# Performance work log

Measured on AMD Instinct MI355X. Metric: run time of the kernel, lower is better.

## Reference

```python
import jax, jax.numpy as jnp
from jax import lax
import numpy as np

N, C_IN, C_OUT, H, W, DS = 32, 16, 1, 128, 128, 5
NC = C_OUT * C_IN  # channels fed to DUBlock convs (= out_nc*nc_d[0])


def autocorr(x, ds):
    """x:(N,C,H,W) -> xtx_raw:(N,C,C,2ds-1,2ds-1).
    xtx_raw[n,i,j,u,v] = sum_{h,w} x[n,i,h,w] * xpad[n,j,u+h,v+w]  (zero pad ds-1),
    matching torch cal_xtx (sample-wise conv3d of x with itself)."""
    n, c, h, w = x.shape
    p = ds - 1
    xp = jnp.pad(x, ((0, 0), (0, 0), (p, p), (p, p)))
    rows = []
    for u in range(2 * ds - 1):
        cols = [jnp.einsum('nihw,njhw->nij', x,
                           lax.slice(xp, (0, 0, u, v), (n, c, u + h, v + w)))
                for v in range(2 * ds - 1)]
        rows.append(jnp.stack(cols, axis=-1))
    return jnp.stack(rows, axis=-2)  # (N,C,C,K,K), K=2ds-1


def crosscorr(x, y, ds):
    """x:(N,Ci,H,W), y:(N,Co,H,W) -> xty:(N,Co,Ci,ds,ds)  (torch cal_xty, pad=(ds-1)//2)."""
    n, c, h, w = x.shape
    p = (ds - 1) // 2
    xp = jnp.pad(x, ((0, 0), (0, 0), (p, p), (p, p)))
    rows = []
    for u in range(ds):
        cols = [jnp.einsum('nohw,njhw->noj', y,
                           lax.slice(xp, (0, 0, u, v), (n, c, u + h, v + w)))
                for v in range(ds)]
        rows.append(jnp.stack(cols, axis=-1))
    return jnp.stack(rows, axis=-2)  # (N,Co,Ci,ds,ds)


def assemble_Q(R, ds):
    """Block-Toeplitz assembly. Equivalent to torch's unfold + flip + index permutation:
    Q[n,(i,p,q),(j,oi,oj)] = R[n,i,j, ds-1+oi-p, ds-1+oj-q]."""
    n, c = R.shape[0], R.shape[1]
    r = jnp.arange(ds)
    idx = (ds - 1) + r[None, :] - r[:, None]  # idx[p,o] = ds-1+o-p in [0, 2ds-2]
    Q6 = R[:, :, :, idx[:, None, :, None], idx[None, :, None, :]]  # (N,i,j,p,q,oi,oj)
    return jnp.transpose(Q6, (0, 1, 3, 4, 2, 5, 6)).reshape(n, c * ds * ds, c * ds * ds)


def dsb(x, d, y, alpha, reg):
    """DSBlock: regularized normal equations + batched SPD solve.
    x:(N,Ci,H,W), d:(N,Co,Ci,ds,ds), y:(N,Co,H,W), alpha:(N,1,1,1), reg:(1,)"""
    n, ci, h, w = x.shape
    co, ds = d.shape[1], d.shape[-1]
    Q = assemble_Q(autocorr(x, ds), ds)                               # (N, ci*ds^2, ci*ds^2)
    P = crosscorr(x, y, ds).reshape(n, co, -1).transpose(0, 2, 1)      # (N, ci*ds^2, co)
    a = alpha.reshape(n, 1, 1) * (h * w) * reg / (ds * ds * ci)        # (N,1,1)
    m = Q.shape[1]
    Q = Q + a * jnp.eye(m, dtype=Q.dtype)
    P = P + a * d.reshape(n, co, -1).transpose(0, 2, 1)
    # torch uses cholesky + cholesky_solve on SPD Q; jnp.linalg.solve computes the
    # same solution (and its vjp matches the custom CholeskySolve backward for symmetric Q).
    D = jnp.linalg.solve(Q, P)                                         # (N, ci*ds^2, co)
    return D.reshape(n, ci, ds, ds, co).transpose(0, 4, 1, 2, 3)       # (N,Co,Ci,ds,ds)


def conv3x3(x, wgt, b):
    o = lax.conv_general_dilated(x, wgt, (1, 1), ((1, 1), (1, 1)),
                                 dimension_numbers=('NCHW', 'OIHW', 'NCHW'))
    return o + b[None, :, None, None]


def dblock_fwd(x1, x2, d, y1, y2, alpha, beta, reg,
               w1, b1, w2, b2, w3, b3, w4, b4, w5, b5, w6, b6):
    d = dsb(x1, d, y1, alpha, reg)
    d = dsb(x2, d, y2, alpha, reg)
    n, co, ci, ds = d.shape[0], d.shape[1], d.shape[2], d.shape[3]
    bmap = jnp.broadcast_to(1.0 / jnp.sqrt(beta), (n, 1, ds, ds))      # (1/beta.sqrt()).repeat
    h0 = jnp.concatenate([d.reshape(n, co * ci, ds, ds), bmap], axis=1)
    # DUBlock
    t = jax.nn.relu(conv3x3(jax.nn.relu(conv3x3(h0, w1, b1)), w2, b2))
    t = jax.nn.relu(conv3x3(jax.nn.relu(conv3x3(t, w3, b3)), w4, b4))
    t = conv3x3(jax.nn.relu(conv3x3(t, w5, b5)), w6, b6) + h0[:, :-1]
    return t.reshape(n, co, ci, ds, ds)


def setup_inputs() -> dict:
    key = jax.random.key(0)
    ks = jax.random.split(key, 24)
    inp = {
        'x1': jax.random.normal(ks[0], (N, C_IN, H, W), jnp.float32),
        'x2': jax.random.normal(ks[1], (N, C_IN, H, W), jnp.float32),
        'd': jax.random.normal(ks[2], (N, C_OUT, C_IN, DS, DS), jnp.float32),
        'y1': jax.random.normal(ks[3], (N, C_OUT, H, W), jnp.float32),
        'y2': jax.random.normal(ks[4], (N, C_OUT, H, W), jnp.float32),
        'alpha': jax.random.uniform(ks[5], (N, 1, 1, 1), jnp.float32),
        'beta': jax.random.uniform(ks[6], (N, 1, 1, 1), jnp.float32),
        'reg': jnp.ones((1,), jnp.float32),
    }
    cins = [NC + 1, NC, NC, NC, NC, NC]
    for i in range(6):
        inp['w%d' % (i + 1)] = 0.05 * jax.random.normal(ks[7 + i], (NC, cins[i], 3, 3), jnp.float32)
        inp['b%d' % (i + 1)] = jnp.zeros((NC,), jnp.float32)
    return inp


def reference(x1, x2, d, y1, y2, alpha, beta, reg,
              w1, b1, w2, b2, w3, b3, w4, b4, w5, b5, w6, b6):
    return dblock_fwd(x1, x2, d, y1, y2, alpha, beta, reg,
                      w1, b1, w2, b2, w3, b3, w4, b4, w5, b5, w6, b6)
```

## Files before the change

kernel.cpp:

```cpp
#include <hip/hip_runtime.h>
#include <hip/hip_bf16.h>

constexpr int NS   = 32;
constexpr int C    = 16;
constexpr int H    = 128;
constexpr int W    = 128;
constexpr int DS   = 5;
constexpr int M    = C * DS * DS;
constexpr int NLAG = 81;

typedef short short8 __attribute__((ext_vector_type(8)));
typedef float f32x4 __attribute__((ext_vector_type(4)));

constexpr int CH_U    = 152;
constexpr int SLOT_U  = 16 * CH_U;
constexpr int SLOT_B  = SLOT_U * 2;
constexpr int RING_B  = 16 * SLOT_B;
constexpr int CHK     = 19;
constexpr size_t XB_US_PER_IN = (size_t)NS * H * 16 * CH_U;

constexpr int WREP_F  = 6 * 144 * 20 + 6 * 16;
constexpr int WREP_CH = WREP_F * 4 / 16;

__device__ __forceinline__ unsigned int pk_bf16(float a, float b) {
    union { __hip_bfloat162 h; unsigned int u; } cv;
    cv.h = __float22bfloat162_rn(make_float2(a, b));
    return cv.u;
}

__device__ __forceinline__ void gl_lds16(const void* g, void* l) {
    __builtin_amdgcn_global_load_lds(
        (const __attribute__((address_space(1))) unsigned int*)g,
        (__attribute__((address_space(3))) unsigned int*)l, 16, 0, 0);
}

__global__ __launch_bounds__(256, 1)
void prep_kernel(const float* __restrict__ x1, const float* __restrict__ x2,
                 const float* __restrict__ y1, const float* __restrict__ y2,
                 unsigned short* __restrict__ xb,
                 float* __restrict__ P1, float* __restrict__ P2,
                 const float* __restrict__ w1, const float* __restrict__ b1,
                 const float* __restrict__ w2, const float* __restrict__ b2,
                 const float* __restrict__ w3, const float* __restrict__ b3,
                 const float* __restrict__ w4, const float* __restrict__ b4,
                 const float* __restrict__ w5, const float* __restrict__ b5,
                 const float* __restrict__ w6, const float* __restrict__ b6,
                 float* __restrict__ wrep)
{
    const int b = blockIdx.x, tid = threadIdx.x;
    if (b < 1024) {
        const int n = b & 31, zi = (b >> 5) & 1, rg = b >> 6;
        const float* xn = (zi ? x2 : x1) + (size_t)n * C * H * W;
        uint4* dst = (uint4*)(xb + (size_t)zi * XB_US_PER_IN +
                              ((size_t)n * H) * SLOT_U);
        for (int f = tid; f < 8 * 16 * CHK; f += 256) {
            const int rc = f / CHK, g = f - rc * CHK;
            const int row = rg * 8 + (rc >> 4), ch = rc & 15;
            uint4 o = make_uint4(0u, 0u, 0u, 0u);
            if (g >= 1 && g <= 16) {
                const float4* s4 = (const float4*)(xn + ((size_t)ch * H + row) * W + (g - 1) * 8);
                float4 va = s4[0], vb = s4[1];
                o.x = pk_bf16(va.x, va.y); o.y = pk_bf16(va.z, va.w);
                o.z = pk_bf16(vb.x, vb.y); o.w = pk_bf16(vb.z, vb.w);
            }
            dst[((size_t)row * 16 + ch) * CHK + g] = o;
        }
        return;
    }
    if (b < 2048) {
        const int b2 = b - 1024;
        const int n = b2 & 31, j = (b2 >> 5) & 15, zi = b2 >> 9;
        const float* x = zi ? x2 : x1;
        const float* y = zi ? y2 : y1;
        float* P       = zi ? P2 : P1;

        const float* yn = y + (size_t)n * H * W;
        const float* xc = x + ((size_t)n * C + j) * H * W;

        const int wg = tid & 31, slab = tid >> 5;
        const int r0 = slab * 16;

        float acc[25];
#pragma unroll
        for (int l = 0; l < 25; ++l) acc[l] = 0.f;

        float4 yw[5];
#pragma unroll
        for (int u = 0; u < 5; ++u) {
            const int t = r0 + 1 - u;
            yw[u] = (t >= 0) ? *(const float4*)(yn + (size_t)t * W + wg * 4)
                             : make_float4(0.f, 0.f, 0.f, 0.f);
        }

#pragma unroll 4
        for (int rr = 0; rr < 16; ++rr) {
            const int r = r0 + rr;
#pragma unroll
            for (int u = 4; u >= 1; --u) yw[u] = yw[u - 1];
            const int tnew = r + 2;
            yw[0] = (tnew < H) ? *(const float4*)(yn + (size_t)tnew * W + wg * 4)
                               : make_float4(0.f, 0.f, 0.f, 0.f);

            const float* xr = xc + (size_t)r * W + wg * 4;
            float w12[12];
            float4 t4 = (wg > 0) ? *(const float4*)(xr - 4) : make_float4(0, 0, 0, 0);
            w12[0] = t4.x; w12[1] = t4.y; w12[2] = t4.z; w12[3] = t4.w;
            t4 = *(const float4*)(xr);
            w12[4] = t4.x; w12[5] = t4.y; w12[6] = t4.z; w12[7] = t4.w;
            t4 = (wg < 31) ? *(const float4*)(xr + 4) : make_float4(0, 0, 0, 0);
            w12[8] = t4.x; w12[9] = t4.y; w12[10] = t4.z; w12[11] = t4.w;

#pragma unroll
            for (int u = 0; u < 5; ++u) {
#pragma unroll
                for (int v = 0; v < 5; ++v)
                    acc[u * 5 + v] += yw[u].x * w12[2 + v] + yw[u].y * w12[3 + v] +
                                      yw[u].z * w12[4 + v] + yw[u].w * w12[5 + v];
            }
        }

        __shared__ float red[4][25];
        const int lane = tid & 63, wv = tid >> 6;
#pragma unroll
        for (int l = 0; l < 25; ++l) {
            float v = acc[l];
#pragma unroll
            for (int off = 32; off; off >>= 1) v += __shfl_down(v, off);
            if (lane == 0) red[wv][l] = v;
        }
        __syncthreads();
        if (tid < 25)
            P[((size_t)n * C + j) * 25 + tid] = red[0][tid] + red[1][tid] + red[2][tid] + red[3][tid];
        return;
    }
    const float* wsl[6] = {w1, w2, w3, w4, w5, w6};
    const float* bsl[6] = {b1, b2, b3, b4, b5, b6};
#pragma unroll
    for (int l = 0; l < 6; ++l) {
        const int cin = (l == 0) ? 17 : 16;
        const float* ws = wsl[l];
        for (int f = tid; f < 16 * cin * 9; f += 256) {
            const int o = f / (cin * 9);
            const int rm = f - o * cin * 9;
            const int ci = rm / 9, kk = rm - ci * 9;
            wrep[l * 2880 + (o * 9 + kk) * 20 + ci] = ws[f];
        }
        if (tid < 16) wrep[17280 + l * 16 + tid] = bsl[l][tid];
    }
}

template<int P0, int P1>
__device__ __forceinline__ void autocorr_body(const unsigned short* __restrict__ xn,
                                              float* __restrict__ Rn,
                                              char* sm, int tid)
{
    constexpr int U0 = P0 / 9;
    constexpr int U1 = (P1 - 1) / 9;
    constexpr int NB = U1 - U0 + 1;
    constexpr int NP = P1 - P0;
    constexpr int SLOT_Q = SLOT_B / 16;

    unsigned short* ring = (unsigned short*)sm;
    const int lane = tid & 63;
    const int wid  = tid >> 6;
    const int q    = lane >> 4;
    const int mi   = lane & 15;
    const int rh   = wid & 3;
    const int chh  = wid >> 2;

    f32x4 acc[NP];
#pragma unroll
    for (int l = 0; l < NP; ++l) acc[l] = (f32x4){0.f, 0.f, 0.f, 0.f};

    const char* gb = (const char*)xn;

    for (int f = tid; f < 4 * SLOT_Q; f += 512)
        ((uint4*)sm)[(12 + f / SLOT_Q) * SLOT_Q + (f % SLOT_Q)] = make_uint4(0, 0, 0, 0);
    for (int f = wid; f < 38; f += 8)
        gl_lds16(gb + (size_t)f * 1024 + lane * 16, sm + f * 1024);
    __syncthreads();

    for (int s = 0; s < H; s += 4) {
        if (s < H - 8) {
            const size_t gbase = (size_t)(s + 8) * SLOT_B;
            char* lbase = sm + ((s + 8) & 15) * SLOT_B;
            for (int f = wid; f < 19; f += 8)
                gl_lds16(gb + gbase + (size_t)f * 1024 + lane * 16, lbase + f * 1024);
        } else {
            for (int f = tid; f < 4 * SLOT_Q; f += 512)
                ((uint4*)sm)[(((s + 8 + f / SLOT_Q) & 15)) * SLOT_Q + (f % SLOT_Q)] = make_uint4(0, 0, 0, 0);
        }

        const int r = s + rh;
        const unsigned short* rowA = ring + (r & 15) * SLOT_U + mi * CH_U;
#pragma unroll
        for (int cc = 0; cc < 2; ++cc) {
            const int w0 = (chh * 2 + cc) * 32;
            const uint4* pa = (const uint4*)(rowA + w0 + 8 * q);
            uint4 A0 = pa[0], A1 = pa[1], A2 = pa[2];
            unsigned int d[12] = {A0.x, A0.y, A0.z, A0.w, A1.x, A1.y, A1.z, A1.w,
                                  A2.x, A2.y, A2.z, A2.w};
            short8 bf[NB];
#pragma unroll
            for (int u = U0; u <= U1; ++u)
                bf[u - U0] = *(const short8*)(ring + ((r + u - 4 + 16) & 15) * SLOT_U +
                                              mi * CH_U + 8 + w0 + 8 * q);
#pragma unroll
            for (int v = 0; v < 9; ++v) {
                const int off = 12 - v;
                const int q4  = off >> 1;
                union { unsigned int u4[4]; short8 s8; } af;
                if (off & 1) {
#pragma unroll
                    for (int k2 = 0; k2 < 4; ++k2)
                        af.u4[k2] = (d[q4 + k2] >> 16) | (d[q4 + k2 + 1] << 16);
                } else {
#pragma unroll
                    for (int k2 = 0; k2 < 4; ++k2) af.u4[k2] = d[q4 + k2];
                }
#pragma unroll
                for (int u = U0; u <= U1; ++u) {
                    if (u * 9 + v >= P0 && u * 9 + v < P1)
                        acc[u * 9 + v - P0] = __builtin_amdgcn_mfma_f32_16x16x32_bf16(
                            af.s8, bf[u - U0], acc[u * 9 + v - P0], 0, 0, 0);
                }
            }
        }
        __syncthreads();
    }

    float* sred = (float*)sm;
#pragma unroll
    for (int cb = 0; cb < NP; cb += 9) {
        const int nc = (NP - cb < 9) ? (NP - cb) : 9;
        __syncthreads();
#pragma unroll
        for (int pp = 0; pp < 9; ++pp) {
            if (pp < nc) {
#pragma unroll
                for (int rg = 0; rg < 4; ++rg)
                    sred[(pp * 8 + wid) * 256 + (q * 4 + rg) * 16 + mi] = acc[cb + pp][rg];
            }
        }
        __syncthreads();
        if (tid < 256) {
#pragma unroll
            for (int pp = 0; pp < 9; ++pp) {
                if (pp < nc) {
                    float ssum = 0.f;
#pragma unroll
                    for (int w8 = 0; w8 < 8; ++w8)
                        ssum += sred[(pp * 8 + w8) * 256 + tid];
                    Rn[(size_t)tid * NLAG + P0 + cb + pp] = ssum;
                }
            }
        }
    }
}

__global__ __launch_bounds__(512, 2)
void autocorr_mfma(const unsigned short* __restrict__ xb,
                   float* __restrict__ R1, float* __restrict__ R2)
{
    __shared__ __align__(16) char sm[RING_B];
    const int n = blockIdx.x, zi = blockIdx.y, ug = blockIdx.z;
    const unsigned short* xn = xb + (size_t)zi * XB_US_PER_IN + (size_t)n * H * SLOT_U;
    float* Rn = (zi ? R2 : R1) + (size_t)n * C * C * NLAG;
    switch (ug) {
        case 0:  autocorr_body< 0, 20>(xn, Rn, sm, threadIdx.x); break;
        case 1:  autocorr_body<20, 40>(xn, Rn, sm, threadIdx.x); break;
        case 2:  autocorr_body<40, 60>(xn, Rn, sm, threadIdx.x); break;
        default: autocorr_body<60, 81>(xn, Rn, sm, threadIdx.x); break;
    }
}

__device__ __forceinline__ float block_sum512(float v, float* red, int tid)
{
#pragma unroll
    for (int off = 32; off; off >>= 1) v += __shfl_down(v, off);
    if ((tid & 63) == 0) red[tid >> 6] = v;
    __syncthreads();
    float s = red[0] + red[1] + red[2] + red[3] + red[4] + red[5] + red[6] + red[7];
    __syncthreads();
    return s;
}

__device__ __forceinline__ float2 block_sum512_f2(float v0, float v1, float* red, int tid)
{
#pragma unroll
    for (int off = 32; off; off >>= 1) { v0 += __shfl_down(v0, off); v1 += __shfl_down(v1, off); }
    if ((tid & 63) == 0) { red[(tid >> 6) * 2] = v0; red[(tid >> 6) * 2 + 1] = v1; }
    __syncthreads();
    float s0 = 0.f, s1 = 0.f;
#pragma unroll
    for (int i = 0; i < 8; ++i) { s0 += red[2 * i]; s1 += red[2 * i + 1]; }
    __syncthreads();
    return make_float2(s0, s1);
}

__device__ __forceinline__ float cg_solve(const float (&Rreg)[81], float rhs,
                                          int iters, float a, int t,
                                          float* pv, float* ap, float* red)
{
    const int jj = t & 15;
    float zreg = 0.f, rreg = 0.f, pmine = 0.f;
    if (t < M) {
        rreg = rhs; pmine = rhs;
        pv[(t / 25) * 28 + (t % 25)] = rhs;
    }
    float rr = block_sum512((t < M) ? rreg * rreg : 0.f, red, t);

    for (int it = 0; it < iters; ++it) {
        if (t < 256) {
            float pld[25], acc[25];
            const float* pj = &pv[jj * 28];
#pragma unroll
            for (int k = 0; k < 25; ++k) pld[k] = pj[k];
#pragma unroll
            for (int k = 0; k < 25; ++k) acc[k] = 0.f;
#pragma unroll
            for (int u = 0; u < 9; ++u) {
#pragma unroll
                for (int v = 0; v < 9; ++v) {
                    const float Rv = Rreg[u * 9 + v];
#pragma unroll
                    for (int c = 0; c < 5; ++c) {
                        if (c < u - 4 || c > u) continue;
                        const int aa = 4 + c - u;
#pragma unroll
                        for (int dd = 0; dd < 5; ++dd) {
                            if (dd < v - 4 || dd > v) continue;
                            const int bb = 4 + dd - v;
                            acc[aa * 5 + bb] += Rv * pld[c * 5 + dd];
                        }
                    }
                }
            }
#pragma unroll
            for (int k = 0; k < 25; ++k) {
                float s2 = acc[k];
                s2 += __shfl_down(s2, 8, 16);
                s2 += __shfl_down(s2, 4, 16);
                s2 += __shfl_down(s2, 2, 16);
                s2 += __shfl_down(s2, 1, 16);
                acc[k] = s2;
            }
            if (jj == 0) {
#pragma unroll
                for (int k = 0; k < 25; ++k) ap[(t >> 4) * 25 + k] = acc[k];
            }
        }
        __syncthreads();
        float wv = 0.f;
        if (t < M) wv = ap[t] + a * pmine;
        const float2 dots = block_sum512_f2((t < M) ? pmine * wv : 0.f,
                                            (t < M) ? wv * wv : 0.f, red, t);
        const float pAp = dots.x, ww = dots.y;
        const bool ok = (pAp > 1e-30f);
        const float al  = ok ? rr / pAp : 0.f;
        float rrn = ok ? fmaxf(al * al * ww - rr, 0.f) : rr;
        const float be  = (rr > 1e-30f) ? rrn / rr : 0.f;
        rr = rrn;
        if (t < M) {
            zreg += al * pmine;
            rreg -= al * wv;
            pmine = rreg + be * pmine;
            pv[(t / 25) * 28 + (t % 25)] = pmine;
        }
        __syncthreads();
    }
    return zreg;
}

__global__ __launch_bounds__(512, 1)
void solve_kernel(const float* __restrict__ R1, const float* __restrict__ R2,
                  const float* __restrict__ P1, const float* __restrict__ P2,
                  const float* __restrict__ d0, const float* __restrict__ alpha,
                  const float* __restrict__ beta, const float* __restrict__ reg,
                  const float* __restrict__ wrep,
                  float* __restrict__ out)
{
    __shared__ __align__(16) float Rl[256 * NLAG];
    __shared__ float pv[16 * 28];
    __shared__ float ap[M];
    __shared__ float red[16];
    __shared__ float h0p[25 * 20];
    __shared__ float bufA[25 * 20], bufB[25 * 20];

    const int n = blockIdx.x, t = threadIdx.x;
    const float a = alpha[n] * (float)(H * W) * reg[0] / (float)(DS * DS * C);

    {
        const char* g = (const char*)(R1 + (size_t)n * 256 * NLAG);
        char* l = (char*)Rl;
        for (int f = t; f < 5184; f += 512)
            gl_lds16(g + (size_t)f * 16, l + (size_t)f * 16);
    }
    float rhs1 = 0.f;
    if (t < M) rhs1 = P1[(size_t)n * M + t] + a * d0[(size_t)n * M + t];
    __syncthreads();

    float Rreg[81];
    {
        const float* Rrow = &Rl[(t & 255) * NLAG];
#pragma unroll
        for (int i = 0; i < 81; ++i) Rreg[i] = Rrow[i];
    }
    __syncthreads();

    {
        const char* g = (const char*)(R2 + (size_t)n * 256 * NLAG);
        char* l = (char*)Rl;
        for (int f = t; f < 5184; f += 512)
            gl_lds16(g + (size_t)f * 16, l + (size_t)f * 16);
    }
    float z1 = cg_solve(Rreg, rhs1, 3, a, t, pv, ap, red);
    {
        const float* Rrow = &Rl[(t & 255) * NLAG];
#pragma unroll
        for (int i = 0; i < 81; ++i) Rreg[i] = Rrow[i];
    }
    __syncthreads();

    {
        const char* g = (const char*)wrep;
        char* l = (char*)Rl;
        for (int f = t; f < WREP_CH; f += 512)
            gl_lds16(g + (size_t)f * 16, l + (size_t)f * 16);
    }
    float rhs2 = 0.f;
    if (t < M) rhs2 = P2[(size_t)n * M + t] + a * z1;
    float z2 = cg_solve(Rreg, rhs2, 7, a, t, pv, ap, red);

    const float* wall = (const float*)Rl;
    if (t < M) h0p[(t % 25) * 20 + t / 25] = z2;
    if (t < 25) h0p[t * 20 + 16] = rsqrtf(beta[n]);
    __syncthreads();

#pragma unroll
    for (int l = 0; l < 6; ++l) {
        const float* act = (l == 0) ? h0p : ((l & 1) ? bufA : bufB);
        float s = 0.f;
        if (t < 400) {
            const int o = t / 25, pix = t % 25, yy = pix / 5, xx = pix % 5;
            s = wall[17280 + l * 16 + o];
#pragma unroll
            for (int ky = 0; ky < 3; ++ky) {
                const int iy = yy + ky - 1;
                if ((unsigned)iy >= 5u) continue;
#pragma unroll
                for (int kx = 0; kx < 3; ++kx) {
                    const int ix = xx + kx - 1;
                    if ((unsigned)ix >= 5u) continue;
                    const float* ip = act + (iy * 5 + ix) * 20;
                    const float* wp = wall + l * 2880 + (o * 9 + ky * 3 + kx) * 20;
                    const float4 a0 = *(const float4*)(ip);
                    const float4 a1 = *(const float4*)(ip + 4);
                    const float4 a2 = *(const float4*)(ip + 8);
                    const float4 a3 = *(const float4*)(ip + 12);
                    const float4 q0 = *(const float4*)(wp);
                    const float4 q1 = *(const float4*)(wp + 4);
                    const float4 q2 = *(const float4*)(wp + 8);
                    const float4 q3 = *(const float4*)(wp + 12);
                    s += a0.x * q0.x + a0.y * q0.y + a0.z * q0.z + a0.w * q0.w
                       + a1.x * q1.x + a1.y * q1.y + a1.z * q1.z + a1.w * q1.w
                       + a2.x * q2.x + a2.y * q2.y + a2.z * q2.z + a2.w * q2.w
                       + a3.x * q3.x + a3.y * q3.y + a3.z * q3.z + a3.w * q3.w;
                    if (l == 0) s += ip[16] * wp[16];
                }
            }
            if (l < 5) s = fmaxf(s, 0.f);
            else       s += h0p[(t % 25) * 20 + t / 25];
        }
        if (t < 400) {
            if (l == 5) out[(size_t)n * M + t] = s;
            else {
                float* dstb = (l & 1) ? bufB : bufA;
                dstb[(t % 25) * 20 + t / 25] = s;
            }
        }
        __syncthreads();
    }
}

extern "C" void kernel_launch(void* const* d_in, const int* in_sizes, int n_in,
                              void* d_out, int out_size, void* d_ws, size_t ws_size,
                              hipStream_t stream)
{
    (void)in_sizes; (void)n_in; (void)out_size; (void)ws_size;
    const float* x1    = (const float*)d_in[0];
    const float* x2    = (const float*)d_in[1];
    const float* d0    = (const float*)d_in[2];
    const float* y1    = (const float*)d_in[3];
    const float* y2    = (const float*)d_in[4];
    const float* alpha = (const float*)d_in[5];
    const float* beta  = (const float*)d_in[6];
    const float* reg   = (const float*)d_in[7];
    const float* w1 = (const float*)d_in[8];  const float* b1 = (const float*)d_in[9];
    const float* w2 = (const float*)d_in[10]; const float* b2 = (const float*)d_in[11];
    const float* w3 = (const float*)d_in[12]; const float* b3 = (const float*)d_in[13];
    const float* w4 = (const float*)d_in[14]; const float* b4 = (const float*)d_in[15];
    const float* w5 = (const float*)d_in[16]; const float* b5 = (const float*)d_in[17];
    const float* w6 = (const float*)d_in[18]; const float* b6 = (const float*)d_in[19];
    float* out = (float*)d_out;

    char* wsb = (char*)d_ws;
    unsigned short* xb = (unsigned short*)wsb;
    float* R1 = (float*)(wsb + 2 * XB_US_PER_IN * 2);
    const size_t RSZ = (size_t)NS * C * C * NLAG;
    float* R2 = R1 + RSZ;
    float* P1 = R2 + RSZ;
    float* P2 = P1 + (size_t)NS * M;
    float* wrep = P2 + (size_t)NS * M;

    prep_kernel<<<2049, 256, 0, stream>>>(x1, x2, y1, y2, xb, P1, P2,
                                          w1, b1, w2, b2, w3, b3, w4, b4,
                                          w5, b5, w6, b6, wrep);
    autocorr_mfma<<<dim3(NS, 2, 4), 512, 0, stream>>>(xb, R1, R2);
    solve_kernel<<<NS, 512, 0, stream>>>(R1, R2, P1, P2, d0, alpha, beta, reg,
                                         wrep, out);
}
```

Before: 291.1 us.

## Shrink solve kernel to 256 threads with two elements per thread

The solve kernel now runs 256 threads instead of 512, and each thread owns two of the 400 CG vector elements. Block reductions now span 4 waves instead of 8. The CG loop is restructured to compute pAp and the residual norm separately, and it skips the final residual/direction update. The pv row padding changes from 28 to 29 to reduce LDS bank conflicts. The aim is to cut barrier and reduction overhead in this latency-bound 32-block kernel, at the cost of more serial work per thread in the elementwise and conv stages.

```diff
diff --git a/kernel.cpp b/kernel.cpp
--- a/kernel.cpp
+++ b/kernel.cpp
@@ -21,6 +21,8 @@
 
 constexpr int WREP_F  = 6 * 144 * 20 + 6 * 16;
 constexpr int WREP_CH = WREP_F * 4 / 16;
+
+constexpr int PVP = 29;
 
 __device__ __forceinline__ unsigned int pk_bf16(float a, float b) {
     union { __hip_bfloat162 h; unsigned int u; } cv;
@@ -274,105 +276,125 @@
     }
 }
 
-__device__ __forceinline__ float block_sum512(float v, float* red, int tid)
+__device__ __forceinline__ float block_sum256(float v, float* red, int t)
 {
 #pragma unroll
     for (int off = 32; off; off >>= 1) v += __shfl_down(v, off);
-    if ((tid & 63) == 0) red[tid >> 6] = v;
-    __syncthreads();
-    float s = red[0] + red[1] + red[2] + red[3] + red[4] + red[5] + red[6] + red[7];
+    if ((t & 63) == 0) red[t >> 6] = v;
+    __syncthreads();
+    float s = red[0] + red[1] + red[2] + red[3];
     __syncthreads();
     return s;
 }
 
-__device__ __forceinline__ float2 block_sum512_f2(float v0, float v1, float* red, int tid)
-{
-#pragma unroll
-    for (int off = 32; off; off >>= 1) { v0 += __shfl_down(v0, off); v1 += __shfl_down(v1, off); }
-    if ((tid & 63) == 0) { red[(tid >> 6) * 2] = v0; red[(tid >> 6) * 2 + 1] = v1; }
-    __syncthreads();
-    float s0 = 0.f, s1 = 0.f;
-#pragma unroll
-    for (int i = 0; i < 8; ++i) { s0 += red[2 * i]; s1 += red[2 * i + 1]; }
-    __syncthreads();
-    return make_float2(s0, s1);
-}
-
-__device__ __forceinline__ float cg_solve(const float (&Rreg)[81], float rhs,
-                                          int iters, float a, int t,
-                                          float* pv, float* ap, float* red)
+__device__ __forceinline__ void cg_solve(const float (&Rreg)[81],
+                                         float rhs0, float rhs1,
+                                         int iters, float a, int t, bool has1,
+                                         float* pv, float* ap, float* red,
+                                         float& z0o, float& z1o)
 {
     const int jj = t & 15;
-    float zreg = 0.f, rreg = 0.f, pmine = 0.f;
-    if (t < M) {
-        rreg = rhs; pmine = rhs;
-        pv[(t / 25) * 28 + (t % 25)] = rhs;
-    }
-    float rr = block_sum512((t < M) ? rreg * rreg : 0.f, red, t);
+    const int e1 = t + 256;
+    float z0 = 0.f, z1 = 0.f;
+    float r0 = rhs0, r1 = has1 ? rhs1 : 0.f;
+    float p0 = r0, p1 = r1;
+    pv[(t / 25) * PVP + (t % 25)] = p0;
+    if (has1) pv[(e1 / 25) * PVP + (e1 % 25)] = p1;
+    float rr = block_sum256(r0 * r0 + r1 * r1, red, t);
 
     for (int it = 0; it < iters; ++it) {
-        if (t < 256) {
-            float pld[25], acc[25];
-            const float* pj = &pv[jj * 28];
-#pragma unroll
-            for (int k = 0; k < 25; ++k) pld[k] = pj[k];
-#pragma unroll
-            for (int k = 0; k < 25; ++k) acc[k] = 0.f;
-#pragma unroll
-            for (int u = 0; u < 9; ++u) {
-#pragma unroll
-                for (int v = 0; v < 9; ++v) {
-                    const float Rv = Rreg[u * 9 + v];
-#pragma unroll
-                    for (int c = 0; c < 5; ++c) {
-                        if (c < u - 4 || c > u) continue;
-                        const int aa = 4 + c - u;
-#pragma unroll
-                        for (int dd = 0; dd < 5; ++dd) {
-                            if (dd < v - 4 || dd > v) continue;
-                            const int bb = 4 + dd - v;
-                            acc[aa * 5 + bb] += Rv * pld[c * 5 + dd];
-                        }
+        float pld[25], acc[25];
+        const float* pj = &pv[jj * PVP];
+#pragma unroll
+        for (int k = 0; k < 25; ++k) pld[k] = pj[k];
+#pragma unroll
+        for (int k = 0; k < 25; ++k) acc[k] = 0.f;
+#pragma unroll
+        for (int u = 0; u < 9; ++u) {
+#pragma unroll
+            for (int v = 0; v < 9; ++v) {
+                const float Rv = Rreg[u * 9 + v];
+#pragma unroll
+                for (int c = 0; c < 5; ++c) {
+                    if (c < u - 4 || c > u) continue;
+                    const int aa = 4 + c - u;
+#pragma unroll
+                    for (int dd = 0; dd < 5; ++dd) {
+                        if (dd < v - 4 || dd > v) continue;
+                        const int bb = 4 + dd - v;
+                        acc[aa * 5 + bb] += Rv * pld[c * 5 + dd];
                     }
                 }
             }
-#pragma unroll
-            for (int k = 0; k < 25; ++k) {
-                float s2 = acc[k];
-                s2 += __shfl_down(s2, 8, 16);
-                s2 += __shfl_down(s2, 4, 16);
-                s2 += __shfl_down(s2, 2, 16);
-                s2 += __shfl_down(s2, 1, 16);
-                acc[k] = s2;
-            }
-            if (jj == 0) {
-#pragma unroll
-                for (int k = 0; k < 25; ++k) ap[(t >> 4) * 25 + k] = acc[k];
-            }
+        }
+#pragma unroll
+        for (int k = 0; k < 25; ++k) {
+            float s2 = acc[k];
+            s2 += __shfl_down(s2, 8, 16);
+            s2 += __shfl_down(s2, 4, 16);
+            s2 += __shfl_down(s2, 2, 16);
+            s2 += __shfl_down(s2, 1, 16);
+            acc[k] = s2;
+        }
+        if (jj == 0) {
+#pragma unroll
+            for (int k = 0; k < 25; ++k) ap[(t >> 4) * 25 + k] = acc[k];
         }
         __syncthreads();
-        float wv = 0.f;
-        if (t < M) wv = ap[t] + a * pmine;
-        const float2 dots = block_sum512_f2((t < M) ? pmine * wv : 0.f,
-                                            (t < M) ? wv * wv : 0.f, red, t);
-        const float pAp = dots.x, ww = dots.y;
-        const bool ok = (pAp > 1e-30f);
-        const float al  = ok ? rr / pAp : 0.f;
-        float rrn = ok ? fmaxf(al * al * ww - rr, 0.f) : rr;
-        const float be  = (rr > 1e-30f) ? rrn / rr : 0.f;
-        rr = rrn;
-        if (t < M) {
-            zreg += al * pmine;
-            rreg -= al * wv;
-            pmine = rreg + be * pmine;
-            pv[(t / 25) * 28 + (t % 25)] = pmine;
-        }
-        __syncthreads();
-    }
-    return zreg;
-}
-
-__global__ __launch_bounds__(512, 1)
+        const float w0 = ap[t] + a * p0;
+        const float w1 = has1 ? (ap[e1] + a * p1) : 0.f;
+        const float pAp = block_sum256(p0 * w0 + p1 * w1, red, t);
+        const float al  = (pAp > 1e-30f) ? rr / pAp : 0.f;
+        z0 += al * p0; z1 += al * p1;
+        if (it + 1 < iters) {
+            r0 -= al * w0; r1 -= al * w1;
+            const float rrn = block_sum256(r0 * r0 + r1 * r1, red, t);
+            const float be  = (rr > 1e-30f) ? rrn / rr : 0.f;
+            rr = rrn;
+            p0 = r0 + be * p0; p1 = r1 + be * p1;
+            pv[(t / 25) * PVP + (t % 25)] = p0;
+            if (has1) pv[(e1 / 25) * PVP + (e1 % 25)] = p1;
+            __syncthreads();
+        }
+    }
+    z0o = z0; z1o = z1;
+}
+
+__device__ __forceinline__ float conv_one(const float* __restrict__ act,
+                                          const float* __restrict__ wall,
+                                          int l, int idx)
+{
+    const int o = idx / 25, pix = idx % 25, yy = pix / 5, xx = pix % 5;
+    float s = wall[17280 + l * 16 + o];
+#pragma unroll
+    for (int ky = 0; ky < 3; ++ky) {
+        const int iy = yy + ky - 1;
+        if ((unsigned)iy >= 5u) continue;
+#pragma unroll
+        for (int kx = 0; kx < 3; ++kx) {
+            const int ix = xx + kx - 1;
+            if ((unsigned)ix >= 5u) continue;
+            const float* ip = act + (iy * 5 + ix) * 20;
+            const float* wp = wall + l * 2880 + (o * 9 + ky * 3 + kx) * 20;
+            const float4 a0 = *(const float4*)(ip);
+            const float4 a1 = *(const float4*)(ip + 4);
+            const float4 a2 = *(const float4*)(ip + 8);
+            const float4 a3 = *(const float4*)(ip + 12);
+            const float4 q0 = *(const float4*)(wp);
+            const float4 q1 = *(const float4*)(wp + 4);
+            const float4 q2 = *(const float4*)(wp + 8);
+            const float4 q3 = *(const float4*)(wp + 12);
+            s += a0.x * q0.x + a0.y * q0.y + a0.z * q0.z + a0.w * q0.w
+               + a1.x * q1.x + a1.y * q1.y + a1.z * q1.z + a1.w * q1.w
+               + a2.x * q2.x + a2.y * q2.y + a2.z * q2.z + a2.w * q2.w
+               + a3.x * q3.x + a3.y * q3.y + a3.z * q3.z + a3.w * q3.w;
+            if (l == 0) s += ip[16] * wp[16];
+        }
+    }
+    return s;
+}
+
+__global__ __launch_bounds__(256, 1)
 void solve_kernel(const float* __restrict__ R1, const float* __restrict__ R2,
                   const float* __restrict__ P1, const float* __restrict__ P2,
                   const float* __restrict__ d0, const float* __restrict__ alpha,
@@ -381,28 +403,30 @@
                   float* __restrict__ out)
 {
     __shared__ __align__(16) float Rl[256 * NLAG];
-    __shared__ float pv[16 * 28];
+    __shared__ float pv[16 * PVP];
     __shared__ float ap[M];
-    __shared__ float red[16];
+    __shared__ float red[8];
     __shared__ float h0p[25 * 20];
     __shared__ float bufA[25 * 20], bufB[25 * 20];
 
     const int n = blockIdx.x, t = threadIdx.x;
+    const bool has1 = (t < M - 256);
+    const int e1 = t + 256;
     const float a = alpha[n] * (float)(H * W) * reg[0] / (float)(DS * DS * C);
 
     {
         const char* g = (const char*)(R1 + (size_t)n * 256 * NLAG);
         char* l = (char*)Rl;
-        for (int f = t; f < 5184; f += 512)
+        for (int f = t; f < 5184; f += 256)
             gl_lds16(g + (size_t)f * 16, l + (size_t)f * 16);
     }
-    float rhs1 = 0.f;
-    if (t < M) rhs1 = P1[(size_t)n * M + t] + a * d0[(size_t)n * M + t];
+    const float rhs10 = P1[(size_t)n * M + t] + a * d0[(size_t)n * M + t];
+    const float rhs11 = has1 ? (P1[(size_t)n * M + e1] + a * d0[(size_t)n * M + e1]) : 0.f;
     __syncthreads();
 
     float Rreg[81];
     {
-        const float* Rrow = &Rl[(t & 255) * NLAG];
+        const float* Rrow = &Rl[t * NLAG];
 #pragma unroll
         for (int i = 0; i < 81; ++i) Rreg[i] = Rrow[i];
     }
@@ -411,12 +435,13 @@
     {
         const char* g = (const char*)(R2 + (size_t)n * 256 * NLAG);
         char* l = (char*)Rl;
-        for (int f = t; f < 5184; f += 512)
+        for (int f = t; f < 5184; f += 256)
             gl_lds16(g + (size_t)f * 16, l + (size_t)f * 16);
     }
-    float z1 = cg_solve(Rreg, rhs1, 3, a, t, pv, ap, red);
+    float z1a, z1b;
+    cg_solve(Rreg, rhs10, rhs11, 3, a, t, has1, pv, ap, red, z1a, z1b);
     {
-        const float* Rrow = &Rl[(t & 255) * NLAG];
+        const float* Rrow = &Rl[t * NLAG];
 #pragma unroll
         for (int i = 0; i < 81; ++i) Rreg[i] = Rrow[i];
     }
@@ -425,59 +450,37 @@
     {
         const char* g = (const char*)wrep;
         char* l = (char*)Rl;
-        for (int f = t; f < WREP_CH; f += 512)
+        for (int f = t; f < WREP_CH; f += 256)
             gl_lds16(g + (size_t)f * 16, l + (size_t)f * 16);
     }
-    float rhs2 = 0.f;
-    if (t < M) rhs2 = P2[(size_t)n * M + t] + a * z1;
-    float z2 = cg_solve(Rreg, rhs2, 7, a, t, pv, ap, red);
+    const float rhs20 = P2[(size_t)n * M + t] + a * z1a;
+    const float rhs21 = has1 ? (P2[(size_t)n * M + e1] + a * z1b) : 0.f;
+    float z20, z21;
+    cg_solve(Rreg, rhs20, rhs21, 7, a, t, has1, pv, ap, red, z20, z21);
 
     const float* wall = (const float*)Rl;
-    if (t < M) h0p[(t % 25) * 20 + t / 25] = z2;
+    h0p[(t % 25) * 20 + t / 25] = z20;
+    if (has1) h0p[(e1 % 25) * 20 + e1 / 25] = z21;
     if (t < 25) h0p[t * 20 + 16] = rsqrtf(beta[n]);
     __syncthreads();
 
 #pragma unroll
     for (int l = 0; l < 6; ++l) {
         const float* act = (l == 0) ? h0p : ((l & 1) ? bufA : bufB);
-        float s = 0.f;
-        if (t < 400) {
-            const int o = t / 25, pix = t % 25, yy = pix / 5, xx = pix % 5;
-            s = wall[17280 + l * 16 + o];
-#pragma unroll
-            for (int ky = 0; ky < 3; ++ky) {
-                const int iy = yy + ky - 1;
-                if ((unsigned)iy >= 5u) continue;
-#pragma unroll
-                for (int kx = 0; kx < 3; ++kx) {
-                    const int ix = xx + kx - 1;
-                    if ((unsigned)ix >= 5u) continue;
-                    const float* ip = act + (iy * 5 + ix) * 20;
-                    const float* wp = wall + l * 2880 + (o * 9 + ky * 3 + kx) * 20;
-                    const float4 a0 = *(const float4*)(ip);
-                    const float4 a1 = *(const float4*)(ip + 4);
-                    const float4 a2 = *(const float4*)(ip + 8);
-                    const float4 a3 = *(const float4*)(ip + 12);
-                    const float4 q0 = *(const float4*)(wp);
-                    const float4 q1 = *(const float4*)(wp + 4);
-                    const float4 q2 = *(const float4*)(wp + 8);
-                    const float4 q3 = *(const float4*)(wp + 12);
-                    s += a0.x * q0.x + a0.y * q0.y + a0.z * q0.z + a0.w * q0.w
-                       + a1.x * q1.x + a1.y * q1.y + a1.z * q1.z + a1.w * q1.w
-                       + a2.x * q2.x + a2.y * q2.y + a2.z * q2.z + a2.w * q2.w
-                       + a3.x * q3.x + a3.y * q3.y + a3.z * q3.z + a3.w * q3.w;
-                    if (l == 0) s += ip[16] * wp[16];
-                }
-            }
-            if (l < 5) s = fmaxf(s, 0.f);
-            else       s += h0p[(t % 25) * 20 + t / 25];
-        }
-        if (t < 400) {
-            if (l == 5) out[(size_t)n * M + t] = s;
-            else {
-                float* dstb = (l & 1) ? bufB : bufA;
-                dstb[(t % 25) * 20 + t / 25] = s;
-            }
+        float s0 = conv_one(act, wall, l, t);
+        float s1 = has1 ? conv_one(act, wall, l, e1) : 0.f;
+        if (l < 5) { s0 = fmaxf(s0, 0.f); s1 = fmaxf(s1, 0.f); }
+        else {
+            s0 += h0p[(t % 25) * 20 + t / 25];
+            if (has1) s1 += h0p[(e1 % 25) * 20 + e1 / 25];
+        }
+        if (l == 5) {
+            out[(size_t)n * M + t] = s0;
+            if (has1) out[(size_t)n * M + e1] = s1;
+        } else {
+            float* dstb = (l & 1) ? bufB : bufA;
+            dstb[(t % 25) * 20 + t / 25] = s0;
+            if (has1) dstb[(e1 % 25) * 20 + e1 / 25] = s1;
         }
         __syncthreads();
     }
@@ -517,6 +520,6 @@
                                           w1, b1, w2, b2, w3, b3, w4, b4,
                                           w5, b5, w6, b6, wrep);
     autocorr_mfma<<<dim3(NS, 2, 4), 512, 0, stream>>>(xb, R1, R2);
-    solve_kernel<<<NS, 512, 0, stream>>>(R1, R2, P1, P2, d0, alpha, beta, reg,
+    solve_kernel<<<NS, 256, 0, stream>>>(R1, R2, P1, P2, d0, alpha, beta, reg,
                                          wrep, out);
 }
```

Result: faster. 263.5 us (-9.5%).
